# Kernel optimization log

Measured on AMD Instinct MI355X. Metric: run time of the kernel, lower is better.

Reference implementation:

```python
import jax, jax.numpy as jnp
import numpy as np

B, R, S, L, H, A, TD = 4, 8, 8, 256, 768, 256, 100


def setup_inputs() -> dict:
    key = jax.random.key(0)
    ks = iter(jax.random.split(key, 64))
    n = lambda *s: jax.random.normal(next(ks), s, jnp.float32)
    p = lambda *s: jax.random.normal(next(ks), s, jnp.float32) * 0.02
    inp = {
        'X': n(B, L, H),
        'X_mean': n(B, H),
        'mask': jnp.ones((B, L), jnp.float32),
        'sk': jax.random.randint(next(ks), (B, R, S, 2), 0, L, dtype=jnp.int32),
        'sk_mask': jnp.ones((B, R, S), jnp.float32),
        'semantic_rel_emb': n(R, H),
        'transe_rel_emb': n(R, TD),
    }
    # 4 EntityExtractors (reconstructed as two H->1 linears producing start/end logits)
    for pref in ('fh', 'bt', 'ft', 'bh'):
        inp[pref + '_ws'] = p(H); inp[pref + '_bs'] = p()
        inp[pref + '_we'] = p(H); inp[pref + '_be'] = p()
    # 2 RelationAttentions (fwd: rel_dim=H, bwd: rel_dim=TD)
    for pref, rd in (('fra', H), ('bra', TD)):
        inp[pref + '_Wx'] = p(H, A);  inp[pref + '_bx'] = p(A)
        inp[pref + '_Wr'] = p(rd, A); inp[pref + '_br'] = p(A)
        inp[pref + '_Wg'] = p(H, A);  inp[pref + '_bg'] = p(A)
        inp[pref + '_V'] = p(A);      inp[pref + '_bv'] = p()
    # 2 FuseExtractors
    for pref in ('ffe', 'bfe'):
        inp[pref + '_Ws'] = p(H, H); inp[pref + '_bs'] = p(H)
        inp[pref + '_Wx'] = p(H, H); inp[pref + '_bx'] = p(H)
    return inp


def _entity(h, ws, bs, we, be):
    # EntityExtractor: start/end logits over last (H) axis
    return jnp.einsum('...h,h->...', h, ws) + bs, jnp.einsum('...h,h->...', h, we) + be


def _rel_attn(X, rel, g, Wx, bx, Wr, br, Wg, bg, V, bv):
    wx = X @ Wx + bx          # (B,L,A)
    wr = rel @ Wr + br        # (R,A)
    wg = g @ Wg + bg          # (B,A)
    z = jnp.tanh(wx[:, None, :, :] + wr[None, :, None, :] + wg[:, None, None, :])  # (B,R,L,A)
    e = jnp.einsum('brla,a->brl', z, V) + bv
    a = jax.nn.softmax(e, axis=-1)                       # (B,R,L)
    c = jnp.einsum('brl,blh->brh', a, X)                 # (B,R,H)
    return c, a


def _sk_to_embeddings(sk, sk_mask, X):
    # vectorized span-endpoint gather + average (replaces B*R*S python loop)
    b_idx = jnp.arange(X.shape[0])[:, None, None]        # (B,1,1)
    emb = (X[b_idx, sk[..., 0]] + X[b_idx, sk[..., 1]]) * 0.5   # (B,R,S,H)
    return sk_mask[..., None] * emb


def _fuse(X, c, sk_embs, sk_mask, Ws, bs, Wx, bx):
    w_x = X @ Wx + bx                                    # (B,L,H)
    w_sk = (sk_embs @ Ws + bs) * sk_mask[..., None]      # (B,R,S,H)
    # h_ijk = Ws*sk + Wx*x_i + c_j + x_i  -> (B,R,S,L,H)
    return (w_sk[:, :, :, None, :] + w_x[:, None, None, :, :]
            + c[:, :, None, None, :] + X[:, None, None, :, :])


def reference(X, X_mean, mask, sk, sk_mask, semantic_rel_emb, transe_rel_emb,
              fh_ws, fh_bs, fh_we, fh_be, bt_ws, bt_bs, bt_we, bt_be,
              ft_ws, ft_bs, ft_we, ft_be, bh_ws, bh_bs, bh_we, bh_be,
              fra_Wx, fra_bx, fra_Wr, fra_br, fra_Wg, fra_bg, fra_V, fra_bv,
              bra_Wx, bra_bx, bra_Wr, bra_br, bra_Wg, bra_bg, bra_V, bra_bv,
              ffe_Ws, ffe_bs, ffe_Wx, ffe_bx, bfe_Ws, bfe_bs, bfe_Wx, bfe_bx):
    fh_s, fh_e = _entity(X, fh_ws, fh_bs, fh_we, fh_be)      # (B,L)
    bt_s, bt_e = _entity(X, bt_ws, bt_bs, bt_we, bt_be)      # (B,L)
    fwd_c, _ = _rel_attn(X, semantic_rel_emb, X_mean,
                         fra_Wx, fra_bx, fra_Wr, fra_br, fra_Wg, fra_bg, fra_V, fra_bv)
    bwd_c, _ = _rel_attn(X, transe_rel_emb, X_mean,
                         bra_Wx, bra_bx, bra_Wr, bra_br, bra_Wg, bra_bg, bra_V, bra_bv)
    sk_embs = _sk_to_embeddings(sk, sk_mask, X)              # (B,R,S,H)
    fwd_hijk = _fuse(X, fwd_c, sk_embs, sk_mask, ffe_Ws, ffe_bs, ffe_Wx, ffe_bx)
    bwd_hijk = _fuse(X, bwd_c, sk_embs, sk_mask, bfe_Ws, bfe_bs, bfe_Wx, bfe_bx)
    ft_s, ft_e = _entity(fwd_hijk, ft_ws, ft_bs, ft_we, ft_be)  # (B,R,S,L)
    bh_s, bh_e = _entity(bwd_hijk, bh_ws, bh_bs, bh_we, bh_be)  # (B,R,S,L)
    return (fh_s, fh_e, bt_s, bt_e, ft_s, ft_e, bh_s, bh_e)
```

## Files before the change

kernel.cpp:

```cpp
#include <hip/hip_runtime.h>
#include <hip/hip_bf16.h>

#define NB 4
#define NR 8
#define NS 8
#define NL 256
#define NH 768
#define NA 256
#define NTD 100

#define WX_F 0
#define WX_B (WX_F + NB*NL*NA)
#define WR_F (WX_B + NB*NL*NA)
#define WR_B (WR_F + NR*NA)
#define WG_F (WR_B + NR*NA)
#define WG_B (WG_F + NB*NA)
#define C_F  (WG_B + NB*NA)
#define C_B  (C_F + NB*NR*NH)
#define QV   (C_B + NB*NR*NH)
#define SCAL (QV + 8*NH)
#define DXL  (SCAL + 8)
#define D1   (DXL + 4*NB*NL)
#define D3   (D1 + 4*NB*NR*NS)
#define ATT  (D3 + 4*NB*NR)
#define XB   (ATT + 2*NB*NR*NL)
#define WT   (XB + (NB*NL*NH)/2)

#define O_FT_S 4096
#define O_FT_E 69632
#define O_BH_S 135168
#define O_BH_E 200704

typedef __attribute__((ext_vector_type(8))) short short8;
typedef __attribute__((ext_vector_type(4))) float f32x4;

struct bh4 { __hip_bfloat16 a, b, c, d; };

__device__ __forceinline__ float tanh_fast(float x) {
    x = fminf(15.f, fmaxf(-15.f, x));
    float t = __expf(2.f * x);
    return (t - 1.f) / (t + 1.f);
}

__device__ __forceinline__ float wave_reduce(float v) {
    #pragma unroll
    for (int off = 32; off > 0; off >>= 1) v += __shfl_down(v, off);
    return v;
}

__global__ void __launch_bounds__(256) k_cvt(const float* __restrict__ X,
                      const float* __restrict__ fra_Wx, const float* __restrict__ bra_Wx,
                      float* __restrict__ ws) {
    __hip_bfloat16* xb = (__hip_bfloat16*)(ws + XB);
    __hip_bfloat16* wt = (__hip_bfloat16*)(ws + WT);
    const int bid = blockIdx.x, tid = threadIdx.x;
    if (bid < 768) {
        const int i0 = bid*1024 + tid*4;
        const float4 v = *(const float4*)(X + i0);
        bh4 o = { __float2bfloat16(v.x), __float2bfloat16(v.y),
                  __float2bfloat16(v.z), __float2bfloat16(v.w) };
        *(bh4*)(xb + i0) = o;
    } else {
        __shared__ float sh[32][33];
        const int t2 = bid - 768;
        const int mt = t2 / 192;
        const int tile = t2 % 192;
        const int h0 = (tile >> 3) * 32, c0 = (tile & 7) * 32;
        const float* W = mt ? bra_Wx : fra_Wx;
        const int r = tid >> 5, c = tid & 31;
        #pragma unroll
        for (int i = 0; i < 4; ++i) {
            const int row = r + 8*i;
            sh[row][c] = W[(size_t)(h0 + row)*NA + c0 + c];
        }
        __syncthreads();
        const int cw = tid >> 5, hw = tid & 31;
        #pragma unroll
        for (int i = 0; i < 4; ++i) {
            const int col = cw + 8*i;
            wt[(size_t)(mt*NA + c0 + col)*NH + h0 + hw] = __float2bfloat16(sh[hw][col]);
        }
    }
}

__global__ void __launch_bounds__(512) k_pre(const float* __restrict__ sem, const float* __restrict__ transe,
                      const float* __restrict__ X_mean,
                      const float* __restrict__ fra_Wr, const float* __restrict__ fra_br,
                      const float* __restrict__ fra_Wg, const float* __restrict__ fra_bg,
                      const float* __restrict__ bra_Wr, const float* __restrict__ bra_br,
                      const float* __restrict__ bra_Wg, const float* __restrict__ bra_bg,
                      const float* __restrict__ ffe_Ws, const float* __restrict__ ffe_bs,
                      const float* __restrict__ ffe_Wx, const float* __restrict__ ffe_bx,
                      const float* __restrict__ bfe_Ws, const float* __restrict__ bfe_bs,
                      const float* __restrict__ bfe_Wx, const float* __restrict__ bfe_bx,
                      const float* __restrict__ ft_ws, const float* __restrict__ ft_we,
                      const float* __restrict__ bh_ws, const float* __restrict__ bh_we,
                      float* __restrict__ ws) {
    __shared__ float sh[768];
    __shared__ float red2[512];
    const int bid = blockIdx.x, tid = threadIdx.x;

    if (bid < 24) {
        const float* s; const float* W; const float* bias; float* out; int K;
        if (bid < 8)       { s = sem + bid*NH;         W = fra_Wr; bias = fra_br; out = ws + WR_F + bid*NA;      K = NH;  }
        else if (bid < 16) { s = transe + (bid-8)*NTD; W = bra_Wr; bias = bra_br; out = ws + WR_B + (bid-8)*NA;  K = NTD; }
        else if (bid < 20) { s = X_mean + (bid-16)*NH; W = fra_Wg; bias = fra_bg; out = ws + WG_F + (bid-16)*NA; K = NH;  }
        else               { s = X_mean + (bid-20)*NH; W = bra_Wg; bias = bra_bg; out = ws + WG_B + (bid-20)*NA; K = NH;  }
        for (int j = tid; j < K; j += 512) sh[j] = s[j];
        __syncthreads();
        const int half = tid >> 8, col = tid & 255;
        const int khalf = (K/2) & ~15;
        const int k0 = half ? khalf : 0, k1 = half ? K : khalf;
        const float* Wc = W + col;
        float acc = 0.f;
        int k = k0;
        for (; k + 16 <= k1; k += 16) {
            float wb[16];
            #pragma unroll
            for (int i = 0; i < 16; ++i) wb[i] = Wc[(size_t)(k+i)*NA];
            #pragma unroll
            for (int i = 0; i < 16; ++i) acc += sh[k+i] * wb[i];
        }
        for (; k < k1; ++k) acc += sh[k] * Wc[(size_t)k*NA];
        red2[half*256 + col] = acc;
        __syncthreads();
        if (half == 0) out[col] = red2[col] + red2[256 + col] + bias[col];
    } else if (bid < 32) {
        const float* a; const float* b2;
        switch (bid - 24) {
            case 0: a = ffe_bs; b2 = ft_ws; break;
            case 1: a = ffe_bs; b2 = ft_we; break;
            case 2: a = ffe_bx; b2 = ft_ws; break;
            case 3: a = ffe_bx; b2 = ft_we; break;
            case 4: a = bfe_bs; b2 = bh_ws; break;
            case 5: a = bfe_bs; b2 = bh_we; break;
            case 6: a = bfe_bx; b2 = bh_ws; break;
            default: a = bfe_bx; b2 = bh_we; break;
        }
        float p = a[tid]*b2[tid];
        if (tid < 256) p += a[tid+512]*b2[tid+512];
        red2[tid] = p; __syncthreads();
        for (int s2 = 256; s2 > 0; s2 >>= 1) { if (tid < s2) red2[tid] += red2[tid + s2]; __syncthreads(); }
        if (tid == 0) ws[SCAL + (bid - 24)] = red2[0];
    } else {
        const int idx = bid - 32;
        const int mi = idx / 96;
        const int row = (idx % 96)*8 + (tid >> 6);
        const int lane = tid & 63;
        const float* M; const float* v0; const float* v1; bool self;
        switch (mi) {
            case 0: M = ffe_Ws; v0 = ft_ws; v1 = ft_we; self = false; break;
            case 1: M = bfe_Ws; v0 = bh_ws; v1 = bh_we; self = false; break;
            case 2: M = ffe_Wx; v0 = ft_ws; v1 = ft_we; self = true;  break;
            default: M = bfe_Wx; v0 = bh_ws; v1 = bh_we; self = true; break;
        }
        const float4* mr4 = (const float4*)(M + (size_t)row*NH);
        const float4* va4 = (const float4*)v0;
        const float4* vb4 = (const float4*)v1;
        float a0 = 0.f, a1 = 0.f;
        #pragma unroll
        for (int i = 0; i < 3; ++i) {
            const float4 m4 = mr4[lane + 64*i];
            const float4 x4 = va4[lane + 64*i];
            const float4 y4 = vb4[lane + 64*i];
            a0 += m4.x*x4.x + m4.y*x4.y + m4.z*x4.z + m4.w*x4.w;
            a1 += m4.x*y4.x + m4.y*y4.y + m4.z*y4.z + m4.w*y4.w;
        }
        a0 = wave_reduce(a0); a1 = wave_reduce(a1);
        if (lane == 0) {
            ws[QV + (mi*2 + 0)*NH + row] = a0 + (self ? v0[row] : 0.f);
            ws[QV + (mi*2 + 1)*NH + row] = a1 + (self ? v1[row] : 0.f);
        }
    }
}

__global__ void __launch_bounds__(256) k_wx(const float* __restrict__ fra_bx,
                                            const float* __restrict__ bra_bx,
                                            float* __restrict__ ws) {
    const __hip_bfloat16* xb = (const __hip_bfloat16*)(ws + XB);
    const __hip_bfloat16* wt = (const __hip_bfloat16*)(ws + WT);
    const int bid = blockIdx.x, tid = threadIdx.x;
    const int fb = bid >> 8;
    const int rt = (bid & 255) >> 2, cg = bid & 3;
    const int wv = tid >> 6, lane = tid & 63;
    const int m0 = rt * 16, c0 = cg * 64 + wv * 16;
    const int r16 = lane & 15, koff = (lane >> 4) * 8;

    const short8* ap = (const short8*)(xb + (size_t)(m0 + r16)*NH + koff);
    const short8* bp = (const short8*)(wt + (size_t)(fb*NA + c0 + r16)*NH + koff);

    f32x4 acc = {0.f, 0.f, 0.f, 0.f};
    #pragma unroll
    for (int ks = 0; ks < 24; ks += 4) {
        short8 a0 = ap[(ks+0)*4], b0 = bp[(ks+0)*4];
        short8 a1 = ap[(ks+1)*4], b1 = bp[(ks+1)*4];
        short8 a2 = ap[(ks+2)*4], b2 = bp[(ks+2)*4];
        short8 a3 = ap[(ks+3)*4], b3 = bp[(ks+3)*4];
        acc = __builtin_amdgcn_mfma_f32_16x16x32_bf16(a0, b0, acc, 0, 0, 0);
        acc = __builtin_amdgcn_mfma_f32_16x16x32_bf16(a1, b1, acc, 0, 0, 0);
        acc = __builtin_amdgcn_mfma_f32_16x16x32_bf16(a2, b2, acc, 0, 0, 0);
        acc = __builtin_amdgcn_mfma_f32_16x16x32_bf16(a3, b3, acc, 0, 0, 0);
    }
    const float* bia = fb ? bra_bx : fra_bx;
    float* outp = ws + (fb ? WX_B : WX_F);
    const int col = c0 + r16;
    const float bb = bia[col];
    const int rbase = m0 + (lane >> 4) * 4;
    #pragma unroll
    for (int j = 0; j < 4; ++j)
        outp[(size_t)(rbase + j)*NA + col] = acc[j] + bb;
}

__global__ void __launch_bounds__(512) k_attn(const float* __restrict__ fra_V, const float* __restrict__ fra_bv,
                       const float* __restrict__ bra_V, const float* __restrict__ bra_bv,
                       float* __restrict__ ws) {
    __shared__ float wa_s[NA], v_s[NA], red[NL], part[NL];
    const int bid = blockIdx.x, tid = threadIdx.x;
    const int fb = bid >> 5, b = (bid >> 3) & 3, r = bid & 7;
    const int l = tid & 255, half = tid >> 8;

    const float* wr = ws + (fb ? WR_B : WR_F) + r*NA;
    const float* wg = ws + (fb ? WG_B : WG_F) + b*NA;
    const float* V  = fb ? bra_V : fra_V;
    const float  bv = fb ? bra_bv[0] : fra_bv[0];
    const float* wxp = ws + (fb ? WX_B : WX_F);

    if (tid < 256) { wa_s[tid] = wr[tid] + wg[tid]; v_s[tid] = V[tid]; }
    __syncthreads();

    const float4* wxrow = (const float4*)(wxp + (size_t)(b*NL + l)*NA + half*128);
    float acc = 0.f;
    for (int a0 = 0; a0 < 32; a0 += 8) {
        float4 wb[8];
        #pragma unroll
        for (int i = 0; i < 8; ++i) wb[i] = wxrow[a0 + i];
        #pragma unroll
        for (int i = 0; i < 8; ++i) {
            const int a = half*128 + (a0 + i)*4;
            acc += tanh_fast(wb[i].x + wa_s[a+0]) * v_s[a+0];
            acc += tanh_fast(wb[i].y + wa_s[a+1]) * v_s[a+1];
            acc += tanh_fast(wb[i].z + wa_s[a+2]) * v_s[a+2];
            acc += tanh_fast(wb[i].w + wa_s[a+3]) * v_s[a+3];
        }
    }
    if (half) part[l] = acc;
    __syncthreads();

    float e = 0.f;
    if (!half) e = acc + part[l] + bv;
    if (tid < 256) red[tid] = e;
    __syncthreads();
    for (int s2 = 128; s2 > 0; s2 >>= 1) { if (tid < s2) red[tid] = fmaxf(red[tid], red[tid+s2]); __syncthreads(); }
    const float mx = red[0];
    __syncthreads();
    float p = 0.f;
    if (tid < 256) { p = __expf(e - mx); red[tid] = p; }
    __syncthreads();
    for (int s2 = 128; s2 > 0; s2 >>= 1) { if (tid < s2) red[tid] += red[tid+s2]; __syncthreads(); }
    if (tid < 256)
        ws[ATT + ((size_t)(fb*NB + b)*NR + r)*NL + tid] = p / red[0];
}

__global__ void __launch_bounds__(256) k_ctx(const float* __restrict__ X, float* __restrict__ ws) {
    __shared__ float a_s[NL];
    const int bid = blockIdx.x, tid = threadIdx.x;
    const int hc = bid % 3;
    const int r  = (bid / 3) & 7;
    const int b  = (bid / 24) & 3;
    const int fb = bid / 96;

    a_s[tid] = ws[ATT + ((size_t)(fb*NB + b)*NR + r)*NL + tid];
    __syncthreads();

    const float* Xp = X + (size_t)b*NL*NH + hc*256 + tid;
    float c = 0.f;
    for (int l0 = 0; l0 < NL; l0 += 8) {
        float xb_[8];
        #pragma unroll
        for (int i = 0; i < 8; ++i) xb_[i] = Xp[(size_t)(l0+i)*NH];
        #pragma unroll
        for (int i = 0; i < 8; ++i) c += a_s[l0+i] * xb_[i];
    }
    ws[(fb ? C_B : C_F) + (size_t)(b*NR + r)*NH + hc*256 + tid] = c;
}

__global__ void __launch_bounds__(256) k_dxl(const float* __restrict__ X,
                      const float* __restrict__ fh_ws, const float* __restrict__ fh_bs,
                      const float* __restrict__ fh_we, const float* __restrict__ fh_be,
                      const float* __restrict__ bt_ws, const float* __restrict__ bt_bs,
                      const float* __restrict__ bt_we, const float* __restrict__ bt_be,
                      float* __restrict__ ws, float* __restrict__ out) {
    __shared__ float xr[NH];
    const int m = blockIdx.x;
    const int tid = threadIdx.x, w = tid >> 6, lane = tid & 63;

    if (tid < 192) ((float4*)xr)[tid] = ((const float4*)(X + (size_t)m*NH))[tid];
    __syncthreads();

    const float* v0; const float* v1; float add0, add1; float* o0; float* o1;
    if (w == 0)      { v0 = fh_ws; add0 = fh_bs[0]; o0 = out;        v1 = fh_we; add1 = fh_be[0]; o1 = out + 1024; }
    else if (w == 1) { v0 = bt_ws; add0 = bt_bs[0]; o0 = out + 2048; v1 = bt_we; add1 = bt_be[0]; o1 = out + 3072; }
    else if (w == 2) { v0 = ws + QV + 4*NH; add0 = ws[SCAL+2]; o0 = ws + DXL;
                       v1 = ws + QV + 5*NH; add1 = ws[SCAL+3]; o1 = ws + DXL + 1024; }
    else             { v0 = ws + QV + 6*NH; add0 = ws[SCAL+6]; o0 = ws + DXL + 2048;
                       v1 = ws + QV + 7*NH; add1 = ws[SCAL+7]; o1 = ws + DXL + 3072; }

    const float4* xr4 = (const float4*)xr;
    const float4* v04 = (const float4*)v0;
    const float4* v14 = (const float4*)v1;
    float a0 = 0.f, a1 = 0.f;
    #pragma unroll
    for (int i = 0; i < 3; ++i) {
        const float4 x4 = xr4[lane + 64*i];
        const float4 p4 = v04[lane + 64*i];
        const float4 q4 = v14[lane + 64*i];
        a0 += x4.x*p4.x + x4.y*p4.y + x4.z*p4.z + x4.w*p4.w;
        a1 += x4.x*q4.x + x4.y*q4.y + x4.z*q4.z + x4.w*q4.w;
    }
    a0 = wave_reduce(a0); a1 = wave_reduce(a1);
    if (lane == 0) { o0[m] = a0 + add0; o1[m] = a1 + add1; }
}

__global__ void __launch_bounds__(256) k_sk(const float* __restrict__ X, const int* __restrict__ sk,
                     const float* __restrict__ sk_mask,
                     const float* __restrict__ ft_ws, const float* __restrict__ ft_we,
                     const float* __restrict__ bh_ws, const float* __restrict__ bh_we,
                     float* __restrict__ ws) {
    __shared__ float avg[NH];
    const int brs = blockIdx.x;
    const int tid = threadIdx.x, w = tid >> 6, lane = tid & 63;
    const int b = brs >> 6, br = brs >> 3;
    const int i0 = sk[brs*2], i1 = sk[brs*2 + 1];
    const float mk = sk_mask[brs];

    if (tid < 192) {
        const float4 x0 = ((const float4*)(X + (size_t)(b*NL + i0)*NH))[tid];
        const float4 x1 = ((const float4*)(X + (size_t)(b*NL + i1)*NH))[tid];
        float4 o; o.x = 0.5f*(x0.x+x1.x); o.y = 0.5f*(x0.y+x1.y);
        o.z = 0.5f*(x0.z+x1.z); o.w = 0.5f*(x0.w+x1.w);
        ((float4*)avg)[tid] = o;
    }
    __syncthreads();

    const float4* q4 = (const float4*)(ws + QV + w*NH);
    const float4* av4 = (const float4*)avg;
    float acc = 0.f;
    #pragma unroll
    for (int i = 0; i < 3; ++i) {
        const float4 a4 = av4[lane + 64*i];
        const float4 b4 = q4[lane + 64*i];
        acc += a4.x*b4.x + a4.y*b4.y + a4.z*b4.z + a4.w*b4.w;
    }
    acc = wave_reduce(acc);
    if (lane == 0) {
        const float bsdot = ws[SCAL + ((w < 2) ? w : (w + 2))];
        ws[D1 + w*(NB*NR*NS) + brs] = mk*mk*acc + mk*bsdot;
    }

    if ((brs & 7) == 0) {
        const float4* c4 = (const float4*)(ws + ((w < 2) ? C_F : C_B) + (size_t)br*NH);
        const float* v = (w == 0) ? ft_ws : (w == 1) ? ft_we : (w == 2) ? bh_ws : bh_we;
        const float4* vv4 = (const float4*)v;
        float d = 0.f;
        #pragma unroll
        for (int i = 0; i < 3; ++i) {
            const float4 a4 = c4[lane + 64*i];
            const float4 b4 = vv4[lane + 64*i];
            d += a4.x*b4.x + a4.y*b4.y + a4.z*b4.z + a4.w*b4.w;
        }
        d = wave_reduce(d);
        if (lane == 0) ws[D3 + w*(NB*NR) + br] = d;
    }
}

__global__ void __launch_bounds__(256) k_final(const float* __restrict__ ft_bs, const float* __restrict__ ft_be,
                        const float* __restrict__ bh_bs, const float* __restrict__ bh_be,
                        const float* __restrict__ ws, float* __restrict__ out) {
    const int brs = blockIdx.x, l = threadIdx.x;
    const int b = brs >> 6, br = brs >> 3;
    const int m = b*NL + l;
    const int o = brs*NL + l;
    out[O_FT_S + o] = ws[D1 + 0*256 + brs] + ws[DXL + 0*1024 + m] + ws[D3 + 0*32 + br] + ft_bs[0];
    out[O_FT_E + o] = ws[D1 + 1*256 + brs] + ws[DXL + 1*1024 + m] + ws[D3 + 1*32 + br] + ft_be[0];
    out[O_BH_S + o] = ws[D1 + 2*256 + brs] + ws[DXL + 2*1024 + m] + ws[D3 + 2*32 + br] + bh_bs[0];
    out[O_BH_E + o] = ws[D1 + 3*256 + brs] + ws[DXL + 3*1024 + m] + ws[D3 + 3*32 + br] + bh_be[0];
}

extern "C" void kernel_launch(void* const* d_in, const int* in_sizes, int n_in,
                              void* d_out, int out_size, void* d_ws, size_t ws_size,
                              hipStream_t stream) {
    const float* X        = (const float*)d_in[0];
    const float* X_mean   = (const float*)d_in[1];
    const int*   sk       = (const int*)d_in[3];
    const float* sk_mask  = (const float*)d_in[4];
    const float* sem      = (const float*)d_in[5];
    const float* transe   = (const float*)d_in[6];
    const float* fh_ws = (const float*)d_in[7],  *fh_bs = (const float*)d_in[8];
    const float* fh_we = (const float*)d_in[9],  *fh_be = (const float*)d_in[10];
    const float* bt_ws = (const float*)d_in[11], *bt_bs = (const float*)d_in[12];
    const float* bt_we = (const float*)d_in[13], *bt_be = (const float*)d_in[14];
    const float* ft_ws = (const float*)d_in[15], *ft_bs = (const float*)d_in[16];
    const float* ft_we = (const float*)d_in[17], *ft_be = (const float*)d_in[18];
    const float* bh_ws = (const float*)d_in[19], *bh_bs = (const float*)d_in[20];
    const float* bh_we = (const float*)d_in[21], *bh_be = (const float*)d_in[22];
    const float* fra_Wx = (const float*)d_in[23], *fra_bx = (const float*)d_in[24];
    const float* fra_Wr = (const float*)d_in[25], *fra_br = (const float*)d_in[26];
    const float* fra_Wg = (const float*)d_in[27], *fra_bg = (const float*)d_in[28];
    const float* fra_V  = (const float*)d_in[29], *fra_bv = (const float*)d_in[30];
    const float* bra_Wx = (const float*)d_in[31], *bra_bx = (const float*)d_in[32];
    const float* bra_Wr = (const float*)d_in[33], *bra_br = (const float*)d_in[34];
    const float* bra_Wg = (const float*)d_in[35], *bra_bg = (const float*)d_in[36];
    const float* bra_V  = (const float*)d_in[37], *bra_bv = (const float*)d_in[38];
    const float* ffe_Ws = (const float*)d_in[39], *ffe_bs = (const float*)d_in[40];
    const float* ffe_Wx = (const float*)d_in[41], *ffe_bx = (const float*)d_in[42];
    const float* bfe_Ws = (const float*)d_in[43], *bfe_bs = (const float*)d_in[44];
    const float* bfe_Wx = (const float*)d_in[45], *bfe_bx = (const float*)d_in[46];

    float* out = (float*)d_out;
    float* ws  = (float*)d_ws;

    k_cvt<<<dim3(1152), dim3(256), 0, stream>>>(X, fra_Wx, bra_Wx, ws);

    k_pre<<<dim3(416), dim3(512), 0, stream>>>(sem, transe, X_mean,
        fra_Wr, fra_br, fra_Wg, fra_bg, bra_Wr, bra_br, bra_Wg, bra_bg,
        ffe_Ws, ffe_bs, ffe_Wx, ffe_bx, bfe_Ws, bfe_bs, bfe_Wx, bfe_bx,
        ft_ws, ft_we, bh_ws, bh_we, ws);

    k_wx<<<dim3(512), dim3(256), 0, stream>>>(fra_bx, bra_bx, ws);

    k_attn<<<dim3(64), dim3(512), 0, stream>>>(fra_V, fra_bv, bra_V, bra_bv, ws);

    k_ctx<<<dim3(192), dim3(256), 0, stream>>>(X, ws);

    k_dxl<<<dim3(1024), dim3(256), 0, stream>>>(X, fh_ws, fh_bs, fh_we, fh_be,
        bt_ws, bt_bs, bt_we, bt_be, ws, out);

    k_sk<<<dim3(256), dim3(256), 0, stream>>>(X, sk, sk_mask, ft_ws, ft_we, bh_ws, bh_we, ws);

    k_final<<<dim3(256), dim3(256), 0, stream>>>(ft_bs, ft_be, bh_bs, bh_be, ws, out);
}
```

Baseline: 206.8 us.

## Merge eight kernel launches into four fused kernels

Combines the conversion and precompute kernels into one setup kernel. The attention softmax and context reduction now run in the same block, and the dxl dot products become extra blocks of that launch. The sk and final kernels merge, with per-block D1/D3 scalars kept in shared memory. This removes launch overhead and the ATT/D1/D3 workspace round-trips. In exchange, the context reduction has only 64 blocks running serial 256-length loops, which could lengthen the critical path.

```diff
diff --git a/kernel.cpp b/kernel.cpp
--- a/kernel.cpp
+++ b/kernel.cpp
@@ -20,10 +20,7 @@
 #define QV   (C_B + NB*NR*NH)
 #define SCAL (QV + 8*NH)
 #define DXL  (SCAL + 8)
-#define D1   (DXL + 4*NB*NL)
-#define D3   (D1 + 4*NB*NR*NS)
-#define ATT  (D3 + 4*NB*NR)
-#define XB   (ATT + 2*NB*NR*NL)
+#define XB   (DXL + 4*NB*NL)
 #define WT   (XB + (NB*NL*NH)/2)
 
 #define O_FT_S 4096
@@ -48,42 +45,9 @@
     return v;
 }
 
-__global__ void __launch_bounds__(256) k_cvt(const float* __restrict__ X,
+__global__ void __launch_bounds__(512) k_setup(const float* __restrict__ X,
                       const float* __restrict__ fra_Wx, const float* __restrict__ bra_Wx,
-                      float* __restrict__ ws) {
-    __hip_bfloat16* xb = (__hip_bfloat16*)(ws + XB);
-    __hip_bfloat16* wt = (__hip_bfloat16*)(ws + WT);
-    const int bid = blockIdx.x, tid = threadIdx.x;
-    if (bid < 768) {
-        const int i0 = bid*1024 + tid*4;
-        const float4 v = *(const float4*)(X + i0);
-        bh4 o = { __float2bfloat16(v.x), __float2bfloat16(v.y),
-                  __float2bfloat16(v.z), __float2bfloat16(v.w) };
-        *(bh4*)(xb + i0) = o;
-    } else {
-        __shared__ float sh[32][33];
-        const int t2 = bid - 768;
-        const int mt = t2 / 192;
-        const int tile = t2 % 192;
-        const int h0 = (tile >> 3) * 32, c0 = (tile & 7) * 32;
-        const float* W = mt ? bra_Wx : fra_Wx;
-        const int r = tid >> 5, c = tid & 31;
-        #pragma unroll
-        for (int i = 0; i < 4; ++i) {
-            const int row = r + 8*i;
-            sh[row][c] = W[(size_t)(h0 + row)*NA + c0 + c];
-        }
-        __syncthreads();
-        const int cw = tid >> 5, hw = tid & 31;
-        #pragma unroll
-        for (int i = 0; i < 4; ++i) {
-            const int col = cw + 8*i;
-            wt[(size_t)(mt*NA + c0 + col)*NH + h0 + hw] = __float2bfloat16(sh[hw][col]);
-        }
-    }
-}
-
-__global__ void __launch_bounds__(512) k_pre(const float* __restrict__ sem, const float* __restrict__ transe,
+                      const float* __restrict__ sem, const float* __restrict__ transe,
                       const float* __restrict__ X_mean,
                       const float* __restrict__ fra_Wr, const float* __restrict__ fra_br,
                       const float* __restrict__ fra_Wg, const float* __restrict__ fra_bg,
@@ -96,16 +60,43 @@
                       const float* __restrict__ ft_ws, const float* __restrict__ ft_we,
                       const float* __restrict__ bh_ws, const float* __restrict__ bh_we,
                       float* __restrict__ ws) {
-    __shared__ float sh[768];
-    __shared__ float red2[512];
+    __shared__ float smem[2112];
     const int bid = blockIdx.x, tid = threadIdx.x;
 
-    if (bid < 24) {
+    if (bid < 384) {
+        __hip_bfloat16* xb = (__hip_bfloat16*)(ws + XB);
+        const int i0 = bid*2048 + tid*4;
+        const float4 v = *(const float4*)(X + i0);
+        bh4 o = { __float2bfloat16(v.x), __float2bfloat16(v.y),
+                  __float2bfloat16(v.z), __float2bfloat16(v.w) };
+        *(bh4*)(xb + i0) = o;
+    } else if (bid < 576) {
+        __hip_bfloat16* wt = (__hip_bfloat16*)(ws + WT);
+        const int t2 = bid - 384;
+        const int mt = t2 / 96;
+        const int half = tid >> 8, tid2 = tid & 255;
+        const int tile = (t2 % 96)*2 + half;
+        const int h0 = (tile >> 3) * 32, c0 = (tile & 7) * 32;
+        const float* W = mt ? bra_Wx : fra_Wx;
+        float (*sh)[33] = (float(*)[33])(smem + half*1056);
+        const int r = tid2 >> 5, c = tid2 & 31;
+        #pragma unroll
+        for (int i = 0; i < 4; ++i)
+            sh[r + 8*i][c] = W[(size_t)(h0 + r + 8*i)*NA + c0 + c];
+        __syncthreads();
+        const int cw = tid2 >> 5, hw = tid2 & 31;
+        #pragma unroll
+        for (int i = 0; i < 4; ++i)
+            wt[(size_t)(mt*NA + c0 + cw + 8*i)*NH + h0 + hw] = __float2bfloat16(sh[hw][cw + 8*i]);
+    } else if (bid < 600) {
+        float* sh = smem;
+        float* red2 = smem + 768;
+        const int q = bid - 576;
         const float* s; const float* W; const float* bias; float* out; int K;
-        if (bid < 8)       { s = sem + bid*NH;         W = fra_Wr; bias = fra_br; out = ws + WR_F + bid*NA;      K = NH;  }
-        else if (bid < 16) { s = transe + (bid-8)*NTD; W = bra_Wr; bias = bra_br; out = ws + WR_B + (bid-8)*NA;  K = NTD; }
-        else if (bid < 20) { s = X_mean + (bid-16)*NH; W = fra_Wg; bias = fra_bg; out = ws + WG_F + (bid-16)*NA; K = NH;  }
-        else               { s = X_mean + (bid-20)*NH; W = bra_Wg; bias = bra_bg; out = ws + WG_B + (bid-20)*NA; K = NH;  }
+        if (q < 8)       { s = sem + q*NH;         W = fra_Wr; bias = fra_br; out = ws + WR_F + q*NA;      K = NH;  }
+        else if (q < 16) { s = transe + (q-8)*NTD; W = bra_Wr; bias = bra_br; out = ws + WR_B + (q-8)*NA;  K = NTD; }
+        else if (q < 20) { s = X_mean + (q-16)*NH; W = fra_Wg; bias = fra_bg; out = ws + WG_F + (q-16)*NA; K = NH;  }
+        else             { s = X_mean + (q-20)*NH; W = bra_Wg; bias = bra_bg; out = ws + WG_B + (q-20)*NA; K = NH;  }
         for (int j = tid; j < K; j += 512) sh[j] = s[j];
         __syncthreads();
         const int half = tid >> 8, col = tid & 255;
@@ -125,9 +116,11 @@
         red2[half*256 + col] = acc;
         __syncthreads();
         if (half == 0) out[col] = red2[col] + red2[256 + col] + bias[col];
-    } else if (bid < 32) {
+    } else if (bid < 608) {
+        float* red2 = smem;
+        const int q = bid - 600;
         const float* a; const float* b2;
-        switch (bid - 24) {
+        switch (q) {
             case 0: a = ffe_bs; b2 = ft_ws; break;
             case 1: a = ffe_bs; b2 = ft_we; break;
             case 2: a = ffe_bx; b2 = ft_ws; break;
@@ -141,9 +134,9 @@
         if (tid < 256) p += a[tid+512]*b2[tid+512];
         red2[tid] = p; __syncthreads();
         for (int s2 = 256; s2 > 0; s2 >>= 1) { if (tid < s2) red2[tid] += red2[tid + s2]; __syncthreads(); }
-        if (tid == 0) ws[SCAL + (bid - 24)] = red2[0];
+        if (tid == 0) ws[SCAL + q] = red2[0];
     } else {
-        const int idx = bid - 32;
+        const int idx = bid - 608;
         const int mi = idx / 96;
         const int row = (idx % 96)*8 + (tid >> 6);
         const int lane = tid & 63;
@@ -211,122 +204,126 @@
         outp[(size_t)(rbase + j)*NA + col] = acc[j] + bb;
 }
 
-__global__ void __launch_bounds__(512) k_attn(const float* __restrict__ fra_V, const float* __restrict__ fra_bv,
+__global__ void __launch_bounds__(512) k_attn_dxl(const float* __restrict__ X,
+                       const float* __restrict__ fra_V, const float* __restrict__ fra_bv,
                        const float* __restrict__ bra_V, const float* __restrict__ bra_bv,
-                       float* __restrict__ ws) {
-    __shared__ float wa_s[NA], v_s[NA], red[NL], part[NL];
+                       const float* __restrict__ fh_ws, const float* __restrict__ fh_bs,
+                       const float* __restrict__ fh_we, const float* __restrict__ fh_be,
+                       const float* __restrict__ bt_ws, const float* __restrict__ bt_bs,
+                       const float* __restrict__ bt_we, const float* __restrict__ bt_be,
+                       float* __restrict__ ws, float* __restrict__ out) {
+    __shared__ float smem[1536];
     const int bid = blockIdx.x, tid = threadIdx.x;
-    const int fb = bid >> 5, b = (bid >> 3) & 3, r = bid & 7;
-    const int l = tid & 255, half = tid >> 8;
-
-    const float* wr = ws + (fb ? WR_B : WR_F) + r*NA;
-    const float* wg = ws + (fb ? WG_B : WG_F) + b*NA;
-    const float* V  = fb ? bra_V : fra_V;
-    const float  bv = fb ? bra_bv[0] : fra_bv[0];
-    const float* wxp = ws + (fb ? WX_B : WX_F);
-
-    if (tid < 256) { wa_s[tid] = wr[tid] + wg[tid]; v_s[tid] = V[tid]; }
-    __syncthreads();
-
-    const float4* wxrow = (const float4*)(wxp + (size_t)(b*NL + l)*NA + half*128);
-    float acc = 0.f;
-    for (int a0 = 0; a0 < 32; a0 += 8) {
-        float4 wb[8];
+
+    if (bid < 64) {
+        float* wa_s = smem;
+        float* v_s  = smem + 256;
+        float* red  = smem + 512;
+        float* part = smem + 768;
+        float* a_s  = smem + 1024;
+        const int fb = bid >> 5, b = (bid >> 3) & 3, r = bid & 7;
+        const int l = tid & 255, half = tid >> 8;
+
+        const float* wr = ws + (fb ? WR_B : WR_F) + r*NA;
+        const float* wg = ws + (fb ? WG_B : WG_F) + b*NA;
+        const float* V  = fb ? bra_V : fra_V;
+        const float  bv = fb ? bra_bv[0] : fra_bv[0];
+        const float* wxp = ws + (fb ? WX_B : WX_F);
+
+        if (tid < 256) { wa_s[tid] = wr[tid] + wg[tid]; v_s[tid] = V[tid]; }
+        __syncthreads();
+
+        const float4* wxrow = (const float4*)(wxp + (size_t)(b*NL + l)*NA + half*128);
+        float acc = 0.f;
+        for (int a0 = 0; a0 < 32; a0 += 8) {
+            float4 wb[8];
+            #pragma unroll
+            for (int i = 0; i < 8; ++i) wb[i] = wxrow[a0 + i];
+            #pragma unroll
+            for (int i = 0; i < 8; ++i) {
+                const int a = half*128 + (a0 + i)*4;
+                acc += tanh_fast(wb[i].x + wa_s[a+0]) * v_s[a+0];
+                acc += tanh_fast(wb[i].y + wa_s[a+1]) * v_s[a+1];
+                acc += tanh_fast(wb[i].z + wa_s[a+2]) * v_s[a+2];
+                acc += tanh_fast(wb[i].w + wa_s[a+3]) * v_s[a+3];
+            }
+        }
+        if (half) part[l] = acc;
+        __syncthreads();
+
+        float e = 0.f;
+        if (!half) e = acc + part[l] + bv;
+        if (tid < 256) red[tid] = e;
+        __syncthreads();
+        for (int s2 = 128; s2 > 0; s2 >>= 1) { if (tid < s2) red[tid] = fmaxf(red[tid], red[tid+s2]); __syncthreads(); }
+        const float mx = red[0];
+        __syncthreads();
+        float p = 0.f;
+        if (tid < 256) { p = __expf(e - mx); red[tid] = p; }
+        __syncthreads();
+        for (int s2 = 128; s2 > 0; s2 >>= 1) { if (tid < s2) red[tid] += red[tid+s2]; __syncthreads(); }
+        if (tid < 256) a_s[tid] = p / red[0];
+        __syncthreads();
+
+        const float* Xb = X + (size_t)b*NL*NH;
+        float* cc = ws + (fb ? C_B : C_F) + (size_t)(b*NR + r)*NH;
+        for (int h = tid; h < NH; h += 512) {
+            const float* Xp = Xb + h;
+            float c = 0.f;
+            for (int l0 = 0; l0 < NL; l0 += 8) {
+                float xb_[8];
+                #pragma unroll
+                for (int i = 0; i < 8; ++i) xb_[i] = Xp[(size_t)(l0+i)*NH];
+                #pragma unroll
+                for (int i = 0; i < 8; ++i) c += a_s[l0+i] * xb_[i];
+            }
+            cc[h] = c;
+        }
+    } else {
+        float* xr = smem;
+        const int idx = bid - 64;
+        const int m0 = idx * 2;
+        const int g = tid >> 6, lane = tid & 63;
+        const int row = g >> 2, w = g & 3;
+        const int m = m0 + row;
+
+        if (tid < 384) ((float4*)xr)[tid] = ((const float4*)(X + (size_t)m0*NH))[tid];
+        __syncthreads();
+
+        const float* v0; const float* v1; float add0, add1; float* o0; float* o1;
+        if (w == 0)      { v0 = fh_ws; add0 = fh_bs[0]; o0 = out;        v1 = fh_we; add1 = fh_be[0]; o1 = out + 1024; }
+        else if (w == 1) { v0 = bt_ws; add0 = bt_bs[0]; o0 = out + 2048; v1 = bt_we; add1 = bt_be[0]; o1 = out + 3072; }
+        else if (w == 2) { v0 = ws + QV + 4*NH; add0 = ws[SCAL+2]; o0 = ws + DXL;
+                           v1 = ws + QV + 5*NH; add1 = ws[SCAL+3]; o1 = ws + DXL + 1024; }
+        else             { v0 = ws + QV + 6*NH; add0 = ws[SCAL+6]; o0 = ws + DXL + 2048;
+                           v1 = ws + QV + 7*NH; add1 = ws[SCAL+7]; o1 = ws + DXL + 3072; }
+
+        const float4* xr4 = (const float4*)(xr + row*NH);
+        const float4* v04 = (const float4*)v0;
+        const float4* v14 = (const float4*)v1;
+        float a0 = 0.f, a1 = 0.f;
         #pragma unroll
-        for (int i = 0; i < 8; ++i) wb[i] = wxrow[a0 + i];
-        #pragma unroll
-        for (int i = 0; i < 8; ++i) {
-            const int a = half*128 + (a0 + i)*4;
-            acc += tanh_fast(wb[i].x + wa_s[a+0]) * v_s[a+0];
-            acc += tanh_fast(wb[i].y + wa_s[a+1]) * v_s[a+1];
-            acc += tanh_fast(wb[i].z + wa_s[a+2]) * v_s[a+2];
-            acc += tanh_fast(wb[i].w + wa_s[a+3]) * v_s[a+3];
-        }
-    }
-    if (half) part[l] = acc;
-    __syncthreads();
-
-    float e = 0.f;
-    if (!half) e = acc + part[l] + bv;
-    if (tid < 256) red[tid] = e;
-    __syncthreads();
-    for (int s2 = 128; s2 > 0; s2 >>= 1) { if (tid < s2) red[tid] = fmaxf(red[tid], red[tid+s2]); __syncthreads(); }
-    const float mx = red[0];
-    __syncthreads();
-    float p = 0.f;
-    if (tid < 256) { p = __expf(e - mx); red[tid] = p; }
-    __syncthreads();
-    for (int s2 = 128; s2 > 0; s2 >>= 1) { if (tid < s2) red[tid] += red[tid+s2]; __syncthreads(); }
-    if (tid < 256)
-        ws[ATT + ((size_t)(fb*NB + b)*NR + r)*NL + tid] = p / red[0];
-}
-
-__global__ void __launch_bounds__(256) k_ctx(const float* __restrict__ X, float* __restrict__ ws) {
-    __shared__ float a_s[NL];
-    const int bid = blockIdx.x, tid = threadIdx.x;
-    const int hc = bid % 3;
-    const int r  = (bid / 3) & 7;
-    const int b  = (bid / 24) & 3;
-    const int fb = bid / 96;
-
-    a_s[tid] = ws[ATT + ((size_t)(fb*NB + b)*NR + r)*NL + tid];
-    __syncthreads();
-
-    const float* Xp = X + (size_t)b*NL*NH + hc*256 + tid;
-    float c = 0.f;
-    for (int l0 = 0; l0 < NL; l0 += 8) {
-        float xb_[8];
-        #pragma unroll
-        for (int i = 0; i < 8; ++i) xb_[i] = Xp[(size_t)(l0+i)*NH];
-        #pragma unroll
-        for (int i = 0; i < 8; ++i) c += a_s[l0+i] * xb_[i];
-    }
-    ws[(fb ? C_B : C_F) + (size_t)(b*NR + r)*NH + hc*256 + tid] = c;
-}
-
-__global__ void __launch_bounds__(256) k_dxl(const float* __restrict__ X,
-                      const float* __restrict__ fh_ws, const float* __restrict__ fh_bs,
-                      const float* __restrict__ fh_we, const float* __restrict__ fh_be,
-                      const float* __restrict__ bt_ws, const float* __restrict__ bt_bs,
-                      const float* __restrict__ bt_we, const float* __restrict__ bt_be,
-                      float* __restrict__ ws, float* __restrict__ out) {
-    __shared__ float xr[NH];
-    const int m = blockIdx.x;
-    const int tid = threadIdx.x, w = tid >> 6, lane = tid & 63;
-
-    if (tid < 192) ((float4*)xr)[tid] = ((const float4*)(X + (size_t)m*NH))[tid];
-    __syncthreads();
-
-    const float* v0; const float* v1; float add0, add1; float* o0; float* o1;
-    if (w == 0)      { v0 = fh_ws; add0 = fh_bs[0]; o0 = out;        v1 = fh_we; add1 = fh_be[0]; o1 = out + 1024; }
-    else if (w == 1) { v0 = bt_ws; add0 = bt_bs[0]; o0 = out + 2048; v1 = bt_we; add1 = bt_be[0]; o1 = out + 3072; }
-    else if (w == 2) { v0 = ws + QV + 4*NH; add0 = ws[SCAL+2]; o0 = ws + DXL;
-                       v1 = ws + QV + 5*NH; add1 = ws[SCAL+3]; o1 = ws + DXL + 1024; }
-    else             { v0 = ws + QV + 6*NH; add0 = ws[SCAL+6]; o0 = ws + DXL + 2048;
-                       v1 = ws + QV + 7*NH; add1 = ws[SCAL+7]; o1 = ws + DXL + 3072; }
-
-    const float4* xr4 = (const float4*)xr;
-    const float4* v04 = (const float4*)v0;
-    const float4* v14 = (const float4*)v1;
-    float a0 = 0.f, a1 = 0.f;
-    #pragma unroll
-    for (int i = 0; i < 3; ++i) {
-        const float4 x4 = xr4[lane + 64*i];
-        const float4 p4 = v04[lane + 64*i];
-        const float4 q4 = v14[lane + 64*i];
-        a0 += x4.x*p4.x + x4.y*p4.y + x4.z*p4.z + x4.w*p4.w;
-        a1 += x4.x*q4.x + x4.y*q4.y + x4.z*q4.z + x4.w*q4.w;
-    }
-    a0 = wave_reduce(a0); a1 = wave_reduce(a1);
-    if (lane == 0) { o0[m] = a0 + add0; o1[m] = a1 + add1; }
-}
-
-__global__ void __launch_bounds__(256) k_sk(const float* __restrict__ X, const int* __restrict__ sk,
+        for (int i = 0; i < 3; ++i) {
+            const float4 x4 = xr4[lane + 64*i];
+            const float4 p4 = v04[lane + 64*i];
+            const float4 q4 = v14[lane + 64*i];
+            a0 += x4.x*p4.x + x4.y*p4.y + x4.z*p4.z + x4.w*p4.w;
+            a1 += x4.x*q4.x + x4.y*q4.y + x4.z*q4.z + x4.w*q4.w;
+        }
+        a0 = wave_reduce(a0); a1 = wave_reduce(a1);
+        if (lane == 0) { o0[m] = a0 + add0; o1[m] = a1 + add1; }
+    }
+}
+
+__global__ void __launch_bounds__(256) k_skf(const float* __restrict__ X, const int* __restrict__ sk,
                      const float* __restrict__ sk_mask,
-                     const float* __restrict__ ft_ws, const float* __restrict__ ft_we,
-                     const float* __restrict__ bh_ws, const float* __restrict__ bh_we,
-                     float* __restrict__ ws) {
+                     const float* __restrict__ ft_ws, const float* __restrict__ ft_bs,
+                     const float* __restrict__ ft_we, const float* __restrict__ ft_be,
+                     const float* __restrict__ bh_ws, const float* __restrict__ bh_bs,
+                     const float* __restrict__ bh_we, const float* __restrict__ bh_be,
+                     const float* __restrict__ ws, float* __restrict__ out) {
     __shared__ float avg[NH];
+    __shared__ float d1_s[4], d3_s[4];
     const int brs = blockIdx.x;
     const int tid = threadIdx.x, w = tid >> 6, lane = tid & 63;
     const int b = brs >> 6, br = brs >> 3;
@@ -344,46 +341,32 @@
 
     const float4* q4 = (const float4*)(ws + QV + w*NH);
     const float4* av4 = (const float4*)avg;
-    float acc = 0.f;
+    const float4* c4 = (const float4*)(ws + ((w < 2) ? C_F : C_B) + (size_t)br*NH);
+    const float* v = (w == 0) ? ft_ws : (w == 1) ? ft_we : (w == 2) ? bh_ws : bh_we;
+    const float4* vv4 = (const float4*)v;
+    float acc = 0.f, d = 0.f;
     #pragma unroll
     for (int i = 0; i < 3; ++i) {
         const float4 a4 = av4[lane + 64*i];
         const float4 b4 = q4[lane + 64*i];
+        const float4 e4 = c4[lane + 64*i];
+        const float4 f4 = vv4[lane + 64*i];
         acc += a4.x*b4.x + a4.y*b4.y + a4.z*b4.z + a4.w*b4.w;
-    }
-    acc = wave_reduce(acc);
+        d   += e4.x*f4.x + e4.y*f4.y + e4.z*f4.z + e4.w*f4.w;
+    }
+    acc = wave_reduce(acc); d = wave_reduce(d);
     if (lane == 0) {
         const float bsdot = ws[SCAL + ((w < 2) ? w : (w + 2))];
-        ws[D1 + w*(NB*NR*NS) + brs] = mk*mk*acc + mk*bsdot;
-    }
-
-    if ((brs & 7) == 0) {
-        const float4* c4 = (const float4*)(ws + ((w < 2) ? C_F : C_B) + (size_t)br*NH);
-        const float* v = (w == 0) ? ft_ws : (w == 1) ? ft_we : (w == 2) ? bh_ws : bh_we;
-        const float4* vv4 = (const float4*)v;
-        float d = 0.f;
-        #pragma unroll
-        for (int i = 0; i < 3; ++i) {
-            const float4 a4 = c4[lane + 64*i];
-            const float4 b4 = vv4[lane + 64*i];
-            d += a4.x*b4.x + a4.y*b4.y + a4.z*b4.z + a4.w*b4.w;
-        }
-        d = wave_reduce(d);
-        if (lane == 0) ws[D3 + w*(NB*NR) + br] = d;
-    }
-}
-
-__global__ void __launch_bounds__(256) k_final(const float* __restrict__ ft_bs, const float* __restrict__ ft_be,
-                        const float* __restrict__ bh_bs, const float* __restrict__ bh_be,
-                        const float* __restrict__ ws, float* __restrict__ out) {
-    const int brs = blockIdx.x, l = threadIdx.x;
-    const int b = brs >> 6, br = brs >> 3;
-    const int m = b*NL + l;
-    const int o = brs*NL + l;
-    out[O_FT_S + o] = ws[D1 + 0*256 + brs] + ws[DXL + 0*1024 + m] + ws[D3 + 0*32 + br] + ft_bs[0];
-    out[O_FT_E + o] = ws[D1 + 1*256 + brs] + ws[DXL + 1*1024 + m] + ws[D3 + 1*32 + br] + ft_be[0];
-    out[O_BH_S + o] = ws[D1 + 2*256 + brs] + ws[DXL + 2*1024 + m] + ws[D3 + 2*32 + br] + bh_bs[0];
-    out[O_BH_E + o] = ws[D1 + 3*256 + brs] + ws[DXL + 3*1024 + m] + ws[D3 + 3*32 + br] + bh_be[0];
+        d1_s[w] = mk*mk*acc + mk*bsdot;
+        d3_s[w] = d;
+    }
+    __syncthreads();
+
+    const int l = tid, m = b*NL + l, o = brs*NL + l;
+    out[O_FT_S + o] = d1_s[0] + ws[DXL + 0*1024 + m] + d3_s[0] + ft_bs[0];
+    out[O_FT_E + o] = d1_s[1] + ws[DXL + 1*1024 + m] + d3_s[1] + ft_be[0];
+    out[O_BH_S + o] = d1_s[2] + ws[DXL + 2*1024 + m] + d3_s[2] + bh_bs[0];
+    out[O_BH_E + o] = d1_s[3] + ws[DXL + 3*1024 + m] + d3_s[3] + bh_be[0];
 }
 
 extern "C" void kernel_launch(void* const* d_in, const int* in_sizes, int n_in,
@@ -419,23 +402,16 @@
     float* out = (float*)d_out;
     float* ws  = (float*)d_ws;
 
-    k_cvt<<<dim3(1152), dim3(256), 0, stream>>>(X, fra_Wx, bra_Wx, ws);
-
-    k_pre<<<dim3(416), dim3(512), 0, stream>>>(sem, transe, X_mean,
+    k_setup<<<dim3(992), dim3(512), 0, stream>>>(X, fra_Wx, bra_Wx, sem, transe, X_mean,
         fra_Wr, fra_br, fra_Wg, fra_bg, bra_Wr, bra_br, bra_Wg, bra_bg,
         ffe_Ws, ffe_bs, ffe_Wx, ffe_bx, bfe_Ws, bfe_bs, bfe_Wx, bfe_bx,
         ft_ws, ft_we, bh_ws, bh_we, ws);
 
     k_wx<<<dim3(512), dim3(256), 0, stream>>>(fra_bx, bra_bx, ws);
 
-    k_attn<<<dim3(64), dim3(512), 0, stream>>>(fra_V, fra_bv, bra_V, bra_bv, ws);
-
-    k_ctx<<<dim3(192), dim3(256), 0, stream>>>(X, ws);
-
-    k_dxl<<<dim3(1024), dim3(256), 0, stream>>>(X, fh_ws, fh_bs, fh_we, fh_be,
-        bt_ws, bt_bs, bt_we, bt_be, ws, out);
-
-    k_sk<<<dim3(256), dim3(256), 0, stream>>>(X, sk, sk_mask, ft_ws, ft_we, bh_ws, bh_we, ws);
-
-    k_final<<<dim3(256), dim3(256), 0, stream>>>(ft_bs, ft_be, bh_bs, bh_be, ws, out);
-}
+    k_attn_dxl<<<dim3(576), dim3(512), 0, stream>>>(X, fra_V, fra_bv, bra_V, bra_bv,
+        fh_ws, fh_bs, fh_we, fh_be, bt_ws, bt_bs, bt_we, bt_be, ws, out);
+
+    k_skf<<<dim3(256), dim3(256), 0, stream>>>(X, sk, sk_mask,
+        ft_ws, ft_bs, ft_we, ft_be, bh_ws, bh_bs, bh_we, bh_be, ws, out);
+}
```

Result: slower. 251.2 us (+21.4%).
